# Optimization experiments

Hardware: AMD Instinct MI355X
Metric: run time of the kernel (lower is better)

Reference implementation:

```python
import jax, jax.numpy as jnp
import numpy as np

D_MODEL = 1024
D = 256
B, T = 64, 512


def setup_inputs() -> dict:
    key = jax.random.key(0)
    ks = jax.random.split(key, 7)
    s = 1.0 / np.sqrt(D_MODEL)
    return {
        "x": jax.random.normal(ks[0], (B, T, D_MODEL), dtype=jnp.float32),
        "Wq": jax.random.uniform(ks[1], (D_MODEL, D), jnp.float32, -s, s),
        "bq": jax.random.uniform(ks[2], (D,), jnp.float32, -s, s),
        "Wk": jax.random.uniform(ks[3], (D_MODEL, D), jnp.float32, -s, s),
        "bk": jax.random.uniform(ks[4], (D,), jnp.float32, -s, s),
        "Wv": jax.random.uniform(ks[5], (D_MODEL, D), jnp.float32, -s, s),
        "bv": jax.random.uniform(ks[6], (D,), jnp.float32, -s, s),
    }


def reference(x, Wq, bq, Wk, bk, Wv, bv):
    # Linear projections: [B,T,d_model] -> [B,T,d]
    q = x @ Wq + bq
    k = x @ Wk + bk
    v = x @ Wv + bv
    Tq = x.shape[1]
    scale = k.shape[-1] ** (-0.5)
    # scores: [B,T,T]
    scores = jnp.einsum('bqd,bkd->bqk', q, k) * scale
    causal = jnp.tril(jnp.ones((Tq, Tq), dtype=bool))
    scores = jnp.where(causal, scores, -jnp.inf)
    weights = jax.nn.softmax(scores, axis=-1)
    out = jnp.einsum('bqk,bkd->bqd', weights, v)
    return out
```

## Files before the change

### kernel.cpp

```cpp
#include <hip/hip_runtime.h>
#include <hip/hip_bf16.h>

typedef __attribute__((ext_vector_type(8))) short short8;
typedef __attribute__((ext_vector_type(4))) float floatx4;

#define GLOAD_LDS16(src, dst) \
  __builtin_amdgcn_global_load_lds((const __attribute__((address_space(1))) unsigned int*)(src), \
      (__attribute__((address_space(3))) unsigned int*)(dst), 16, 0, 0)

__device__ __forceinline__ short f2bf(float f) {
    __hip_bfloat16 h = __float2bfloat16(f);
    return *reinterpret_cast<short*>(&h);
}

__device__ __forceinline__ floatx4 mfma16(short8 a, short8 b, floatx4 c) {
    return __builtin_amdgcn_mfma_f32_16x16x32_bf16(a, b, c, 0, 0, 0);
}

__global__ __launch_bounds__(256) void wconv_kernel(const float* __restrict__ Wq,
                                                    const float* __restrict__ Wk,
                                                    const float* __restrict__ Wv,
                                                    __hip_bfloat16* __restrict__ WT) {
    int n = blockIdx.x;
    const float* W = (n < 256) ? Wq : (n < 512 ? Wk : Wv);
    int nl = n & 255;
    __hip_bfloat16* dst = WT + (size_t)n * 1024;
    for (int kk = threadIdx.x; kk < 1024; kk += 256)
        dst[kk] = __float2bfloat16(W[(size_t)kk * 256 + nl]);
}

__global__ __launch_bounds__(256) void proj_kernel(const float* __restrict__ x,
                                                   const __hip_bfloat16* __restrict__ WT,
                                                   const float* __restrict__ bq,
                                                   const float* __restrict__ bk,
                                                   const float* __restrict__ bv,
                                                   __hip_bfloat16* __restrict__ qo,
                                                   __hip_bfloat16* __restrict__ ko,
                                                   __hip_bfloat16* __restrict__ vo) {
    __shared__ __align__(16) __hip_bfloat16 As[128 * 64];
    __shared__ __align__(16) __hip_bfloat16 Bs[128 * 64];
    char* AsB = (char*)As;
    char* BsB = (char*)Bs;

    const int tid = threadIdx.x;
    const int bid = blockIdx.x;
    const int wgid = (bid & 7) * 192 + (bid >> 3);
    const int ntile = wgid % 6;
    const int m0 = (wgid / 6) * 128;
    const int n0 = ntile * 128;
    const int wid = tid >> 6, lane = tid & 63;
    const int wr = wid >> 1, wc = wid & 1;
    const int l15 = lane & 15, lg = lane >> 4;

    floatx4 acc[4][4];
#pragma unroll
    for (int i = 0; i < 4; ++i)
#pragma unroll
        for (int j = 0; j < 4; ++j) acc[i][j] = (floatx4){0.f, 0.f, 0.f, 0.f};

    const int arow = tid >> 3;
    const int acolb = (tid & 7) * 16;

    for (int kt = 0; kt < 16; ++kt) {
#pragma unroll
        for (int s = 0; s < 4; ++s) {
            int o = s * 4096 + tid * 16;
            int row = o >> 7;
            int so = o ^ ((row & 7) << 4);
            const __hip_bfloat16* src = WT + (size_t)(n0 + row) * 1024 + kt * 64 + ((so & 127) >> 1);
            GLOAD_LDS16(src, BsB + o);
        }
#pragma unroll
        for (int s = 0; s < 4; ++s) {
            int row = s * 32 + arow;
            const float* src = x + (size_t)(m0 + row) * 1024 + kt * 64 + (acolb >> 1);
            floatx4 f0 = *(const floatx4*)src;
            floatx4 f1 = *(const floatx4*)(src + 4);
            short8 h;
            h[0] = f2bf(f0[0]); h[1] = f2bf(f0[1]); h[2] = f2bf(f0[2]); h[3] = f2bf(f0[3]);
            h[4] = f2bf(f1[0]); h[5] = f2bf(f1[1]); h[6] = f2bf(f1[2]); h[7] = f2bf(f1[3]);
            int o = row * 128 + (acolb ^ ((row & 7) << 4));
            *(short8*)(AsB + o) = h;
        }
        __syncthreads();

        short8 af[4][2], bfr[4][2];
#pragma unroll
        for (int mt = 0; mt < 4; ++mt) {
            int row = wr * 64 + mt * 16 + l15;
            int rb = row * 128, msk = (row & 7) << 4;
            af[mt][0] = *(const short8*)(AsB + rb + ((lg * 16) ^ msk));
            af[mt][1] = *(const short8*)(AsB + rb + ((64 + lg * 16) ^ msk));
        }
#pragma unroll
        for (int nt = 0; nt < 4; ++nt) {
            int row = wc * 64 + nt * 16 + l15;
            int rb = row * 128, msk = (row & 7) << 4;
            bfr[nt][0] = *(const short8*)(BsB + rb + ((lg * 16) ^ msk));
            bfr[nt][1] = *(const short8*)(BsB + rb + ((64 + lg * 16) ^ msk));
        }
#pragma unroll
        for (int ks = 0; ks < 2; ++ks)
#pragma unroll
            for (int mt = 0; mt < 4; ++mt)
#pragma unroll
                for (int nt = 0; nt < 4; ++nt)
                    acc[mt][nt] = mfma16(af[mt][ks], bfr[nt][ks], acc[mt][nt]);
        __syncthreads();
    }

    const int mat = ntile >> 1;
    const float* bias = (mat == 0) ? bq : (mat == 1 ? bk : bv);
    __hip_bfloat16* ob = (mat == 0) ? qo : (mat == 1 ? ko : vo);
    const float scale = (mat == 0) ? 0.09016844005556021f : 1.0f;

#pragma unroll
    for (int nt = 0; nt < 4; ++nt) {
        int c = (ntile & 1) * 128 + wc * 64 + nt * 16 + l15;
        float bval = bias[c];
#pragma unroll
        for (int mt = 0; mt < 4; ++mt) {
            int row = m0 + wr * 64 + mt * 16 + lg * 4;
#pragma unroll
            for (int r = 0; r < 4; ++r)
                ob[(size_t)(row + r) * 256 + c] = __float2bfloat16((acc[mt][nt][r] + bval) * scale);
        }
    }
}

__global__ __launch_bounds__(256) void attn_kernel(const __hip_bfloat16* __restrict__ q,
                                                   const __hip_bfloat16* __restrict__ k,
                                                   const __hip_bfloat16* __restrict__ v,
                                                   float* __restrict__ out) {
    __shared__ __align__(16) __hip_bfloat16 Ks[64 * 256];
    __shared__ __align__(16) __hip_bfloat16 VTs[256 * 64];
    __shared__ __align__(16) __hip_bfloat16 Ps[4][16 * 64];
    char* KsB = (char*)Ks;
    char* VTB = (char*)VTs;

    const int tid = threadIdx.x;
    const int bid = blockIdx.x;
    const int wgid = (bid & 7) * 64 + (bid >> 3);
    const int qb = wgid & 7, b = wgid >> 3;
    const int wid = tid >> 6, lane = tid & 63;
    const int l15 = lane & 15, lg = lane >> 4;
    char* PsB = (char*)(&Ps[wid][0]);

    short8 qf[8];
    const __hip_bfloat16* qrow = q + ((size_t)(b * 512 + qb * 64 + wid * 16 + l15)) * 256;
#pragma unroll
    for (int ks = 0; ks < 8; ++ks) qf[ks] = *(const short8*)(qrow + ks * 32 + lg * 8);

    float m_[4], lsum[4];
    floatx4 o[16];
#pragma unroll
    for (int r = 0; r < 4; ++r) { m_[r] = -1e30f; lsum[r] = 0.f; }
#pragma unroll
    for (int dt = 0; dt < 16; ++dt) o[dt] = (floatx4){0.f, 0.f, 0.f, 0.f};

    const int vkv = lane;
    const int vd0 = wid * 8;

    for (int c = 0; c <= qb; ++c) {
        const size_t kvbase = (size_t)(b * 512 + c * 64) * 256;
#pragma unroll
        for (int s = 0; s < 8; ++s) {
            int o_ = s * 4096 + tid * 16;
            int row = o_ >> 9;
            int so = o_ ^ ((row & 7) << 4);
            const __hip_bfloat16* src = k + kvbase + (size_t)row * 256 + ((so & 511) >> 1);
            GLOAD_LDS16(src, KsB + o_);
        }
#pragma unroll
        for (int it = 0; it < 8; ++it) {
            int dbase = vd0 + it * 32;
            short8 vv = *(const short8*)(v + kvbase + (size_t)vkv * 256 + dbase);
#pragma unroll
            for (int j = 0; j < 8; ++j) {
                int d = dbase + j;
                int addr = (d * 128 + vkv * 2) ^ ((d & 7) << 4);
                *(short*)(VTB + addr) = vv[j];
            }
        }
        __syncthreads();

        floatx4 s4[4];
#pragma unroll
        for (int t = 0; t < 4; ++t) s4[t] = (floatx4){0.f, 0.f, 0.f, 0.f};
#pragma unroll
        for (int ks = 0; ks < 8; ++ks) {
#pragma unroll
            for (int t = 0; t < 4; ++t) {
                int kv = t * 16 + l15;
                short8 kf = *(const short8*)(KsB + kv * 512 + ((ks * 64 + lg * 16) ^ ((kv & 7) << 4)));
                s4[t] = mfma16(qf[ks], kf, s4[t]);
            }
        }
        if (c == qb) {
#pragma unroll
            for (int t = 0; t < 4; ++t) {
                int kvl = t * 16 + l15;
#pragma unroll
                for (int r = 0; r < 4; ++r)
                    if (kvl > wid * 16 + lg * 4 + r) s4[t][r] = -1e30f;
            }
        }
        float pm[4], alpha[4], rs[4];
#pragma unroll
        for (int r = 0; r < 4; ++r)
            pm[r] = fmaxf(fmaxf(s4[0][r], s4[1][r]), fmaxf(s4[2][r], s4[3][r]));
#pragma unroll
        for (int off = 1; off <= 8; off <<= 1)
#pragma unroll
            for (int r = 0; r < 4; ++r) pm[r] = fmaxf(pm[r], __shfl_xor(pm[r], off));
#pragma unroll
        for (int r = 0; r < 4; ++r) {
            float mn = fmaxf(m_[r], pm[r]);
            alpha[r] = exp2f(m_[r] - mn);
            m_[r] = mn;
        }
#pragma unroll
        for (int t = 0; t < 4; ++t)
#pragma unroll
            for (int r = 0; r < 4; ++r) s4[t][r] = exp2f(s4[t][r] - m_[r]);
#pragma unroll
        for (int r = 0; r < 4; ++r) rs[r] = s4[0][r] + s4[1][r] + s4[2][r] + s4[3][r];
#pragma unroll
        for (int off = 1; off <= 8; off <<= 1)
#pragma unroll
            for (int r = 0; r < 4; ++r) rs[r] += __shfl_xor(rs[r], off);
#pragma unroll
        for (int r = 0; r < 4; ++r) lsum[r] = lsum[r] * alpha[r] + rs[r];
#pragma unroll
        for (int dt = 0; dt < 16; ++dt) {
            o[dt][0] *= alpha[0]; o[dt][1] *= alpha[1];
            o[dt][2] *= alpha[2]; o[dt][3] *= alpha[3];
        }
#pragma unroll
        for (int t = 0; t < 4; ++t)
#pragma unroll
            for (int r = 0; r < 4; ++r) {
                int qq = lg * 4 + r;
                int addr = (qq * 128 + (t * 16 + l15) * 2) ^ ((qq & 7) << 4);
                *(short*)(PsB + addr) = f2bf(s4[t][r]);
            }
#pragma unroll
        for (int h = 0; h < 2; ++h) {
            short8 pa = *(const short8*)(PsB + l15 * 128 + ((h * 64 + lg * 16) ^ ((l15 & 7) << 4)));
#pragma unroll
            for (int dt = 0; dt < 16; ++dt) {
                int d = dt * 16 + l15;
                short8 vb = *(const short8*)(VTB + d * 128 + ((h * 64 + lg * 16) ^ ((d & 7) << 4)));
                o[dt] = mfma16(pa, vb, o[dt]);
            }
        }
        __syncthreads();
    }

    float inv[4];
#pragma unroll
    for (int r = 0; r < 4; ++r) inv[r] = 1.0f / lsum[r];
    size_t obase = ((size_t)(b * 512 + qb * 64 + wid * 16 + lg * 4)) * 256 + l15;
#pragma unroll
    for (int dt = 0; dt < 16; ++dt)
#pragma unroll
        for (int r = 0; r < 4; ++r)
            out[obase + (size_t)r * 256 + dt * 16] = o[dt][r] * inv[r];
}

extern "C" void kernel_launch(void* const* d_in, const int* in_sizes, int n_in,
                              void* d_out, int out_size, void* d_ws, size_t ws_size,
                              hipStream_t stream) {
    const float* x  = (const float*)d_in[0];
    const float* Wq = (const float*)d_in[1];
    const float* bq = (const float*)d_in[2];
    const float* Wk = (const float*)d_in[3];
    const float* bk = (const float*)d_in[4];
    const float* Wv = (const float*)d_in[5];
    const float* bv = (const float*)d_in[6];
    float* out = (float*)d_out;

    char* ws = (char*)d_ws;
    __hip_bfloat16* WT = (__hip_bfloat16*)ws;
    __hip_bfloat16* qo = (__hip_bfloat16*)(ws + (2u << 20));
    __hip_bfloat16* ko = qo + (size_t)32768 * 256;
    __hip_bfloat16* vo = ko + (size_t)32768 * 256;

    wconv_kernel<<<dim3(768), dim3(256), 0, stream>>>(Wq, Wk, Wv, WT);
    proj_kernel<<<dim3(1536), dim3(256), 0, stream>>>(x, WT, bq, bk, bv, qo, ko, vo);
    attn_kernel<<<dim3(512), dim3(256), 0, stream>>>(qo, ko, vo, out);
}
```

Baseline: 158.1 us.

## Pre-convert x to bf16 in a separate pass and load via direct-to-LDS

Adds a standalone kernel that converts the fp32 input x to bf16 in workspace before the projection GEMM. The projection kernel then loads its A tiles with global_load_lds directly into swizzled shared memory, instead of loading fp32 into registers, converting, and storing. This removes per-tile conversion work and register staging from the GEMM and halves its A-operand read bytes. In exchange it adds a full extra pass that reads and writes x, plus one more kernel launch.

```diff
diff --git a/kernel.cpp b/kernel.cpp
--- a/kernel.cpp
+++ b/kernel.cpp
@@ -2,6 +2,7 @@
 #include <hip/hip_bf16.h>
 
 typedef __attribute__((ext_vector_type(8))) short short8;
+typedef __attribute__((ext_vector_type(4))) short short4v;
 typedef __attribute__((ext_vector_type(4))) float floatx4;
 
 #define GLOAD_LDS16(src, dst) \
@@ -15,6 +16,28 @@
 
 __device__ __forceinline__ floatx4 mfma16(short8 a, short8 b, floatx4 c) {
     return __builtin_amdgcn_mfma_f32_16x16x32_bf16(a, b, c, 0, 0, 0);
+}
+
+__global__ __launch_bounds__(256) void xconv_kernel(const float* __restrict__ x,
+                                                    __hip_bfloat16* __restrict__ xb) {
+    const size_t n4 = (size_t)32768 * 1024 / 4;
+    const size_t stride = (size_t)gridDim.x * 256;
+    size_t i = (size_t)blockIdx.x * 256 + threadIdx.x;
+    for (; i + stride < n4; i += 2 * stride) {
+        floatx4 f0 = *(const floatx4*)(x + i * 4);
+        floatx4 f1 = *(const floatx4*)(x + (i + stride) * 4);
+        short4v h0, h1;
+        h0[0] = f2bf(f0[0]); h0[1] = f2bf(f0[1]); h0[2] = f2bf(f0[2]); h0[3] = f2bf(f0[3]);
+        h1[0] = f2bf(f1[0]); h1[1] = f2bf(f1[1]); h1[2] = f2bf(f1[2]); h1[3] = f2bf(f1[3]);
+        *(short4v*)(xb + i * 4) = h0;
+        *(short4v*)(xb + (i + stride) * 4) = h1;
+    }
+    for (; i < n4; i += stride) {
+        floatx4 f = *(const floatx4*)(x + i * 4);
+        short4v h;
+        h[0] = f2bf(f[0]); h[1] = f2bf(f[1]); h[2] = f2bf(f[2]); h[3] = f2bf(f[3]);
+        *(short4v*)(xb + i * 4) = h;
+    }
 }
 
 __global__ __launch_bounds__(256) void wconv_kernel(const float* __restrict__ Wq,
@@ -29,7 +52,7 @@
         dst[kk] = __float2bfloat16(W[(size_t)kk * 256 + nl]);
 }
 
-__global__ __launch_bounds__(256) void proj_kernel(const float* __restrict__ x,
+__global__ __launch_bounds__(256) void proj_kernel(const __hip_bfloat16* __restrict__ xb,
                                                    const __hip_bfloat16* __restrict__ WT,
                                                    const float* __restrict__ bq,
                                                    const float* __restrict__ bk,
@@ -58,9 +81,6 @@
 #pragma unroll
         for (int j = 0; j < 4; ++j) acc[i][j] = (floatx4){0.f, 0.f, 0.f, 0.f};
 
-    const int arow = tid >> 3;
-    const int acolb = (tid & 7) * 16;
-
     for (int kt = 0; kt < 16; ++kt) {
 #pragma unroll
         for (int s = 0; s < 4; ++s) {
@@ -72,15 +92,11 @@
         }
 #pragma unroll
         for (int s = 0; s < 4; ++s) {
-            int row = s * 32 + arow;
-            const float* src = x + (size_t)(m0 + row) * 1024 + kt * 64 + (acolb >> 1);
-            floatx4 f0 = *(const floatx4*)src;
-            floatx4 f1 = *(const floatx4*)(src + 4);
-            short8 h;
-            h[0] = f2bf(f0[0]); h[1] = f2bf(f0[1]); h[2] = f2bf(f0[2]); h[3] = f2bf(f0[3]);
-            h[4] = f2bf(f1[0]); h[5] = f2bf(f1[1]); h[6] = f2bf(f1[2]); h[7] = f2bf(f1[3]);
-            int o = row * 128 + (acolb ^ ((row & 7) << 4));
-            *(short8*)(AsB + o) = h;
+            int o = s * 4096 + tid * 16;
+            int row = o >> 7;
+            int so = o ^ ((row & 7) << 4);
+            const __hip_bfloat16* src = xb + (size_t)(m0 + row) * 1024 + kt * 64 + ((so & 127) >> 1);
+            GLOAD_LDS16(src, AsB + o);
         }
         __syncthreads();
 
@@ -285,8 +301,10 @@
     __hip_bfloat16* qo = (__hip_bfloat16*)(ws + (2u << 20));
     __hip_bfloat16* ko = qo + (size_t)32768 * 256;
     __hip_bfloat16* vo = ko + (size_t)32768 * 256;
-
+    __hip_bfloat16* xb = (__hip_bfloat16*)(ws + 52428800ull);
+
+    xconv_kernel<<<dim3(2048), dim3(256), 0, stream>>>(x, xb);
     wconv_kernel<<<dim3(768), dim3(256), 0, stream>>>(Wq, Wk, Wv, WT);
-    proj_kernel<<<dim3(1536), dim3(256), 0, stream>>>(x, WT, bq, bk, bv, qo, ko, vo);
+    proj_kernel<<<dim3(1536), dim3(256), 0, stream>>>(xb, WT, bq, bk, bv, qo, ko, vo);
     attn_kernel<<<dim3(512), dim3(256), 0, stream>>>(qo, ko, vo, out);
 }
```

Result: slower. 178.4 us (+12.8%).

## Double-buffer projection GEMM with async fp32 x loads into LDS

Applied to the files above, without the earlier changes.

Rewrites the projection GEMM to use 512-thread blocks with 256x128 tiles and a K-step of 32. Loads go through global_load_lds into double-buffered shared memory: x is staged as fp32 and converted to bf16 when fragments are read from LDS. The next tile's loads are issued before the current MFMAs run, and wave priority is raised around the MFMA block. This aims to hide global-load latency behind compute and cut register-staged x loads, but it doubles the LDS traffic for the fp32 A tile and uses about 80KB of LDS per block, which limits occupancy.

```diff
diff --git a/kernel.cpp b/kernel.cpp
--- a/kernel.cpp
+++ b/kernel.cpp
@@ -29,27 +29,25 @@
         dst[kk] = __float2bfloat16(W[(size_t)kk * 256 + nl]);
 }
 
-__global__ __launch_bounds__(256) void proj_kernel(const float* __restrict__ x,
-                                                   const __hip_bfloat16* __restrict__ WT,
-                                                   const float* __restrict__ bq,
-                                                   const float* __restrict__ bk,
-                                                   const float* __restrict__ bv,
-                                                   __hip_bfloat16* __restrict__ qo,
-                                                   __hip_bfloat16* __restrict__ ko,
-                                                   __hip_bfloat16* __restrict__ vo) {
-    __shared__ __align__(16) __hip_bfloat16 As[128 * 64];
-    __shared__ __align__(16) __hip_bfloat16 Bs[128 * 64];
-    char* AsB = (char*)As;
-    char* BsB = (char*)Bs;
+__global__ __launch_bounds__(512, 4) void proj_kernel(const float* __restrict__ x,
+                                                      const __hip_bfloat16* __restrict__ WT,
+                                                      const float* __restrict__ bq,
+                                                      const float* __restrict__ bk,
+                                                      const float* __restrict__ bv,
+                                                      __hip_bfloat16* __restrict__ qo,
+                                                      __hip_bfloat16* __restrict__ ko,
+                                                      __hip_bfloat16* __restrict__ vo) {
+    __shared__ __align__(16) char Ab[2][32768];
+    __shared__ __align__(16) char Bb[2][8192];
 
     const int tid = threadIdx.x;
     const int bid = blockIdx.x;
-    const int wgid = (bid & 7) * 192 + (bid >> 3);
+    const int wgid = (bid & 7) * 96 + (bid >> 3);
     const int ntile = wgid % 6;
-    const int m0 = (wgid / 6) * 128;
+    const int m0 = (wgid / 6) * 256;
     const int n0 = ntile * 128;
     const int wid = tid >> 6, lane = tid & 63;
-    const int wr = wid >> 1, wc = wid & 1;
+    const int wm = wid >> 1, wn = wid & 1;
     const int l15 = lane & 15, lg = lane >> 4;
 
     floatx4 acc[4][4];
@@ -58,69 +56,86 @@
 #pragma unroll
         for (int j = 0; j < 4; ++j) acc[i][j] = (floatx4){0.f, 0.f, 0.f, 0.f};
 
-    const int arow = tid >> 3;
-    const int acolb = (tid & 7) * 16;
-
-    for (int kt = 0; kt < 16; ++kt) {
-#pragma unroll
-        for (int s = 0; s < 4; ++s) {
-            int o = s * 4096 + tid * 16;
-            int row = o >> 7;
-            int so = o ^ ((row & 7) << 4);
-            const __hip_bfloat16* src = WT + (size_t)(n0 + row) * 1024 + kt * 64 + ((so & 127) >> 1);
-            GLOAD_LDS16(src, BsB + o);
-        }
-#pragma unroll
-        for (int s = 0; s < 4; ++s) {
-            int row = s * 32 + arow;
-            const float* src = x + (size_t)(m0 + row) * 1024 + kt * 64 + (acolb >> 1);
-            floatx4 f0 = *(const floatx4*)src;
-            floatx4 f1 = *(const floatx4*)(src + 4);
+#define STAGE_A(KT, BUF) do {                                                        \
+        _Pragma("unroll")                                                            \
+        for (int s = 0; s < 4; ++s) {                                                \
+            int o = s * 8192 + tid * 16;                                             \
+            int row = o >> 7;                                \
+            int sb = (o & 127) ^ ((row & 7) << 4);                                   \
+            const float* src = x + (size_t)(m0 + row) * 1024 + (KT) * 32 + (sb >> 2);\
+            GLOAD_LDS16(src, (BUF) + o);                                             \
+        } } while (0)
+
+#define STAGE_B(KT, BUF) do {                                                        \
+        int o = tid * 16;                                                            \
+        int row = o >> 6;                                     \
+        int so = (o & 63) ^ ((row & 3) << 4);                                        \
+        const __hip_bfloat16* src = WT + (size_t)(n0 + row) * 1024 + (KT) * 32       \
+                                    + (so >> 1);                                     \
+        GLOAD_LDS16(src, (BUF) + o);                                                 \
+    } while (0)
+
+    STAGE_A(0, Ab[0]);
+    STAGE_B(0, Bb[0]);
+    __builtin_amdgcn_sched_barrier(0);
+    asm volatile("s_waitcnt vmcnt(0)" ::: "memory");
+    __builtin_amdgcn_sched_barrier(0);
+    __builtin_amdgcn_s_barrier();
+    __builtin_amdgcn_sched_barrier(0);
+
+    for (int kt = 0; kt < 32; ++kt) {
+        const int cur = kt & 1;
+        if (kt < 31) {
+            STAGE_A(kt + 1, Ab[cur ^ 1]);
+            STAGE_B(kt + 1, Bb[cur ^ 1]);
+        }
+        short8 af[4];
+#pragma unroll
+        for (int mt = 0; mt < 4; ++mt) {
+            int row = wm * 64 + mt * 16 + l15;
+            int rb = row * 128, msk = (row & 7) << 4;
+            floatx4 f0 = *(const floatx4*)(Ab[cur] + rb + ((lg * 32) ^ msk));
+            floatx4 f1 = *(const floatx4*)(Ab[cur] + rb + ((lg * 32 + 16) ^ msk));
             short8 h;
             h[0] = f2bf(f0[0]); h[1] = f2bf(f0[1]); h[2] = f2bf(f0[2]); h[3] = f2bf(f0[3]);
             h[4] = f2bf(f1[0]); h[5] = f2bf(f1[1]); h[6] = f2bf(f1[2]); h[7] = f2bf(f1[3]);
-            int o = row * 128 + (acolb ^ ((row & 7) << 4));
-            *(short8*)(AsB + o) = h;
-        }
-        __syncthreads();
-
-        short8 af[4][2], bfr[4][2];
+            af[mt] = h;
+        }
+        short8 bfr[4];
+#pragma unroll
+        for (int nt = 0; nt < 4; ++nt) {
+            int row = wn * 64 + nt * 16 + l15;
+            bfr[nt] = *(const short8*)(Bb[cur] + row * 64 + ((lg * 16) ^ ((row & 3) << 4)));
+        }
+        __builtin_amdgcn_s_setprio(1);
+#pragma unroll
+        for (int mt = 0; mt < 4; ++mt)
+#pragma unroll
+            for (int nt = 0; nt < 4; ++nt)
+                acc[mt][nt] = mfma16(af[mt], bfr[nt], acc[mt][nt]);
+        __builtin_amdgcn_s_setprio(0);
+        __builtin_amdgcn_sched_barrier(0);
+        asm volatile("s_waitcnt vmcnt(0)" ::: "memory");
+        __builtin_amdgcn_sched_barrier(0);
+        __builtin_amdgcn_s_barrier();
+        __builtin_amdgcn_sched_barrier(0);
+    }
+
+#undef STAGE_B
+#undef STAGE_A
+
+#pragma unroll
+    for (int nt = 0; nt < 4; ++nt) {
+        int g = n0 + wn * 64 + nt * 16 + l15;
+        int mat = g >> 8;
+        const float* bias = (mat == 0) ? bq : (mat == 1 ? bk : bv);
+        __hip_bfloat16* ob = (mat == 0) ? qo : (mat == 1 ? ko : vo);
+        float scale = (mat == 0) ? 0.09016844005556021f : 1.0f;
+        int c = g & 255;
+        float bval = bias[c];
 #pragma unroll
         for (int mt = 0; mt < 4; ++mt) {
-            int row = wr * 64 + mt * 16 + l15;
-            int rb = row * 128, msk = (row & 7) << 4;
-            af[mt][0] = *(const short8*)(AsB + rb + ((lg * 16) ^ msk));
-            af[mt][1] = *(const short8*)(AsB + rb + ((64 + lg * 16) ^ msk));
-        }
-#pragma unroll
-        for (int nt = 0; nt < 4; ++nt) {
-            int row = wc * 64 + nt * 16 + l15;
-            int rb = row * 128, msk = (row & 7) << 4;
-            bfr[nt][0] = *(const short8*)(BsB + rb + ((lg * 16) ^ msk));
-            bfr[nt][1] = *(const short8*)(BsB + rb + ((64 + lg * 16) ^ msk));
-        }
-#pragma unroll
-        for (int ks = 0; ks < 2; ++ks)
-#pragma unroll
-            for (int mt = 0; mt < 4; ++mt)
-#pragma unroll
-                for (int nt = 0; nt < 4; ++nt)
-                    acc[mt][nt] = mfma16(af[mt][ks], bfr[nt][ks], acc[mt][nt]);
-        __syncthreads();
-    }
-
-    const int mat = ntile >> 1;
-    const float* bias = (mat == 0) ? bq : (mat == 1 ? bk : bv);
-    __hip_bfloat16* ob = (mat == 0) ? qo : (mat == 1 ? ko : vo);
-    const float scale = (mat == 0) ? 0.09016844005556021f : 1.0f;
-
-#pragma unroll
-    for (int nt = 0; nt < 4; ++nt) {
-        int c = (ntile & 1) * 128 + wc * 64 + nt * 16 + l15;
-        float bval = bias[c];
-#pragma unroll
-        for (int mt = 0; mt < 4; ++mt) {
-            int row = m0 + wr * 64 + mt * 16 + lg * 4;
+            int row = m0 + wm * 64 + mt * 16 + lg * 4;
 #pragma unroll
             for (int r = 0; r < 4; ++r)
                 ob[(size_t)(row + r) * 256 + c] = __float2bfloat16((acc[mt][nt][r] + bval) * scale);
@@ -287,6 +302,6 @@
     __hip_bfloat16* vo = ko + (size_t)32768 * 256;
 
     wconv_kernel<<<dim3(768), dim3(256), 0, stream>>>(Wq, Wk, Wv, WT);
-    proj_kernel<<<dim3(1536), dim3(256), 0, stream>>>(x, WT, bq, bk, bv, qo, ko, vo);
+    proj_kernel<<<dim3(768), dim3(512), 0, stream>>>(x, WT, bq, bk, bv, qo, ko, vo);
     attn_kernel<<<dim3(512), dim3(256), 0, stream>>>(qo, ko, vo, out);
 }
```

New measurement: 162.1 us. +2.5%, slower.
